# Kernel optimization log

Hardware: AMD Instinct MI355X
Metric: run time of the kernel (lower is better)

Reference implementation:

```python
import jax, jax.numpy as jnp
import numpy as np

INPUT_DIM = 1024; HIDDEN_DIM = 1024; OUTPUT_DIM = 1024
NUM_UNITS = 256; SPARSITY = 0.5
MOTOR = min(HIDDEN_DIM, NUM_UNITS - 4)      # 252 motor (output) neurons
REMAIN = NUM_UNITS - MOTOR                  # 4
COMMAND = max(int(0.4 * REMAIN), 1)         # 1 command neuron
INTER = REMAIN - COMMAND                    # 3 inter neurons
LAYERS = [(INPUT_DIM, INTER), (INTER, COMMAND), (COMMAND, MOTOR)]
B, T = 64, 1024
TS = 1.0  # timespans=None -> unit time step

# NCP-style fixed sparsity masks on ff1/ff2 weights (time_a/time_b unmasked, as in ncps CfCCell)
_rng = np.random.default_rng(0)
MASKS = [jnp.asarray((_rng.random((din + dh, dh)) < (1.0 - SPARSITY)).astype(np.float32)) for din, dh in LAYERS]

PARAM_NAMES = []
for _i in range(3):
    for _n in ('ff1', 'ff2', 'ta', 'tb'):
        PARAM_NAMES += [f'l{_i}_{_n}_w', f'l{_i}_{_n}_b']
PARAM_NAMES += ['hproj_w', 'hproj_b', 'oproj_w', 'oproj_b']


def setup_inputs() -> dict:
    key = jax.random.key(0)
    inp = {'x': jax.random.normal(jax.random.fold_in(key, 100), (B, T, INPUT_DIM), jnp.float32)}
    k = 0
    for i, (din, dh) in enumerate(LAYERS):
        cat = din + dh
        s = 1.0 / np.sqrt(cat)
        for name in ('ff1', 'ff2', 'ta', 'tb'):
            inp[f'l{i}_{name}_w'] = jax.random.uniform(jax.random.fold_in(key, k), (cat, dh), jnp.float32, -s, s); k += 1
            inp[f'l{i}_{name}_b'] = jnp.zeros((dh,), jnp.float32)
    sh = 1.0 / np.sqrt(MOTOR)
    inp['hproj_w'] = jax.random.uniform(jax.random.fold_in(key, 50), (MOTOR, HIDDEN_DIM), jnp.float32, -sh, sh)
    inp['hproj_b'] = jnp.zeros((HIDDEN_DIM,), jnp.float32)
    so = 1.0 / np.sqrt(HIDDEN_DIM)
    inp['oproj_w'] = jax.random.uniform(jax.random.fold_in(key, 51), (HIDDEN_DIM, OUTPUT_DIM), jnp.float32, -so, so)
    inp['oproj_b'] = jnp.zeros((OUTPUT_DIM,), jnp.float32)
    return inp


def _cfc_layer(xin, h, w1, b1, w2, b2, wa, ba, wb, bb, mask):
    # ncps CfCCell mode='default', no backbone: closed-form continuous-time update
    xh = jnp.concatenate([xin, h], axis=-1)
    ff1 = jnp.tanh(xh @ (w1 * mask) + b1)
    ff2 = jnp.tanh(xh @ (w2 * mask) + b2)
    t = jax.nn.sigmoid((xh @ wa + ba) * TS + (xh @ wb + bb))
    return ff1 * (1.0 - t) + t * ff2


def _forward(x, p):
    def step(carry, x_t):
        h0, h1, h2 = carry
        h0 = _cfc_layer(x_t, h0, p['l0_ff1_w'], p['l0_ff1_b'], p['l0_ff2_w'], p['l0_ff2_b'], p['l0_ta_w'], p['l0_ta_b'], p['l0_tb_w'], p['l0_tb_b'], MASKS[0])
        h1 = _cfc_layer(h0, h1, p['l1_ff1_w'], p['l1_ff1_b'], p['l1_ff2_w'], p['l1_ff2_b'], p['l1_ta_w'], p['l1_ta_b'], p['l1_tb_w'], p['l1_tb_b'], MASKS[1])
        h2 = _cfc_layer(h1, h2, p['l2_ff1_w'], p['l2_ff1_b'], p['l2_ff2_w'], p['l2_ff2_b'], p['l2_ta_w'], p['l2_ta_b'], p['l2_tb_w'], p['l2_tb_b'], MASKS[2])
        return (h0, h1, h2), None
    nb = x.shape[0]
    init = (jnp.zeros((nb, INTER), x.dtype), jnp.zeros((nb, COMMAND), x.dtype), jnp.zeros((nb, MOTOR), x.dtype))
    (h0, h1, h2), _ = jax.lax.scan(step, init, jnp.swapaxes(x, 0, 1))  # scan over time
    hx = jnp.concatenate([h0, h1, h2], axis=-1)  # (B, 256) full liquid state
    out = (h2 @ p['hproj_w'] + p['hproj_b']) @ p['oproj_w'] + p['oproj_b']  # motor -> hidden -> output
    return out, hx


def reference(x, l0_ff1_w, l0_ff1_b, l0_ff2_w, l0_ff2_b, l0_ta_w, l0_ta_b, l0_tb_w, l0_tb_b, l1_ff1_w, l1_ff1_b, l1_ff2_w, l1_ff2_b, l1_ta_w, l1_ta_b, l1_tb_w, l1_tb_b, l2_ff1_w, l2_ff1_b, l2_ff2_w, l2_ff2_b, l2_ta_w, l2_ta_b, l2_tb_w, l2_tb_b, hproj_w, hproj_b, oproj_w, oproj_b):
    p = dict(locals())
    x = p.pop('x')
    return _forward(x, p)
```

## Files before the change

kernel.cpp:

```cpp
#include <hip/hip_runtime.h>
#include <stdint.h>

static constexpr uint32_t OFF_MASK  = 0;
static constexpr uint32_t OFF_HID   = 0;
static constexpr uint32_t OFF_W0XT  = 66844;
static constexpr uint32_t OFF_W0H   = 76060;
static constexpr uint32_t OFF_B0    = 76088;
static constexpr uint32_t OFF_W1    = 76100;
static constexpr uint32_t OFF_B1    = 76112;
static constexpr uint32_t OFF_WH2   = 76116;
static constexpr uint32_t OFF_WH1   = 174420;
static constexpr uint32_t OFF_B2    = 175188;
static constexpr uint32_t OFF_XPART = 175948;
static constexpr uint32_t OFF_H2F   = 765772;

struct U128 { uint64_t lo, hi; };
__device__ inline U128 mul128(U128 a, U128 b) {
    U128 r; r.lo = a.lo * b.lo;
    r.hi = a.hi * b.lo + a.lo * b.hi + __umul64hi(a.lo, b.lo);
    return r;
}
__device__ inline U128 add128(U128 a, U128 b) {
    U128 r; r.lo = a.lo + b.lo; r.hi = a.hi + b.hi + (r.lo < b.lo); return r;
}
__device__ inline U128 pcg_mult() { U128 m; m.lo = 0x4385df649fccf645ull; m.hi = 0x2360ed051fc65da4ull; return m; }
__device__ inline void pcg_step(U128& st, U128 inc) { st = add128(mul128(st, pcg_mult()), inc); }

__device__ void pcg_init_np(U128& st, U128& inc) {
    const uint32_t IA = 0x43b0d7e5u, MA = 0x931e8875u, IB = 0x8b51f9ddu, MB = 0x58f38dedu;
    const uint32_t ML = 0xca01f9ddu, MR = 0x4973f715u;
    uint32_t hc = IA;
    auto hmix = [&](uint32_t val) -> uint32_t {
        val ^= hc; hc *= MA; val *= hc; val ^= val >> 16; return val;
    };
    auto mixf = [&](uint32_t x, uint32_t y) -> uint32_t {
        uint32_t r = (x * ML) - (y * MR); r ^= r >> 16; return r;
    };
    uint32_t pool[4];
    for (int i = 0; i < 4; i++) pool[i] = hmix(0u);
    for (int s = 0; s < 4; s++)
        for (int d = 0; d < 4; d++)
            if (s != d) pool[d] = mixf(pool[d], hmix(pool[s]));
    uint32_t hb = IB;
    uint32_t s32[8];
    for (int i = 0; i < 8; i++) {
        uint32_t dv = pool[i & 3];
        dv ^= hb; hb *= MB; dv *= hb; dv ^= dv >> 16;
        s32[i] = dv;
    }
    uint64_t w[4];
    for (int k = 0; k < 4; k++)
        w[k] = (uint64_t)s32[2 * k] | ((uint64_t)s32[2 * k + 1] << 32);
    U128 initstate; initstate.hi = w[0]; initstate.lo = w[1];
    inc.lo = (w[3] << 1) | 1ull;
    inc.hi = (w[2] << 1) | (w[3] >> 63);
    st.lo = 0; st.hi = 0;
    pcg_step(st, inc);
    st = add128(st, initstate);
    pcg_step(st, inc);
}
__device__ inline uint64_t pcg_draw(U128& st, U128 inc) {
    pcg_step(st, inc);
    uint64_t x = st.hi ^ st.lo;
    uint32_t rot = (uint32_t)(st.hi >> 58);
    return (x >> rot) | (x << ((64u - rot) & 63u));
}
__device__ void pcg_advance(U128& st, U128 inc, uint64_t delta) {
    U128 am; am.lo = 1; am.hi = 0;
    U128 ap; ap.lo = 0; ap.hi = 0;
    U128 cm = pcg_mult(), cp = inc;
    while (delta) {
        if (delta & 1) { am = mul128(am, cm); ap = add128(mul128(ap, cm), cp); }
        U128 cm1 = cm; cm1.lo += 1; cm1.hi += (cm1.lo == 0);
        cp = mul128(cm1, cp);
        cm = mul128(cm, cm);
        delta >>= 1;
    }
    st = add128(mul128(st, am), ap);
}

__global__ __launch_bounds__(256) void gen_masks(float* __restrict__ mask) {
    const int tid = threadIdx.x;
    U128 s, inc; pcg_init_np(s, inc);
    pcg_advance(s, inc, (uint64_t)tid * 262u);
    uint32_t base = (uint32_t)tid * 262u;
    for (uint32_t q = 0; q < 262u; q++) {
        uint64_t o = pcg_draw(s, inc);
        uint32_t idx = base + q;
        if (idx < 66841u) mask[idx] = (o >> 63) ? 0.0f : 1.0f;
    }
}

__global__ __launch_bounds__(256) void prep_weights(
    const float* f1w0, const float* f2w0, const float* taw0, const float* tbw0,
    const float* f1b0, const float* f2b0, const float* tab0, const float* tbb0,
    const float* f1w1, const float* f2w1, const float* taw1, const float* tbw1,
    const float* f1b1, const float* f2b1, const float* tab1, const float* tbb1,
    const float* f1w2, const float* f2w2, const float* taw2, const float* tbw2,
    const float* f1b2, const float* f2b2, const float* tab2, const float* tbb2,
    float* ws)
{
    const float* mask = ws + OFF_MASK;
    uint32_t id = blockIdx.x * 256u + threadIdx.x;
    if (id < 98304u) {
        uint32_t m = id / 32768u, r = id % 32768u;
        uint32_t q = r / 1024u, r2 = r % 1024u, jp = r2 >> 2, c = r2 & 3u;
        uint32_t p = q * 4u + c;
        auto wv = [&](uint32_t k) -> float {
            if (m == 0u) return f1w2[k * 252u + jp] * mask[3085u + k * 252u + jp];
            if (m == 1u) return f2w2[k * 252u + jp] * mask[3085u + k * 252u + jp];
            return taw2[k * 252u + jp] + tbw2[k * 252u + jp];
        };
        float a = 0.0f, bb = 0.0f;
        if (jp < 252u && p < 126u) { a = wv(1u + 2u * p); bb = wv(2u + 2u * p); }
        union { uint32_t u; _Float16 h[2]; } pk;
        pk.h[0] = (_Float16)a; pk.h[1] = (_Float16)bb;
        ((uint32_t*)ws)[OFF_WH2 + id] = pk.u;
        return;
    }
    uint32_t t = id - 98304u;
    if (t < 768u) {
        uint32_t mm = t / 256u, jp = t % 256u;
        float v = 0.0f;
        if (jp < 252u) {
            if (mm == 0u)      v = f1w2[jp] * mask[3085u + jp];
            else if (mm == 1u) v = f2w2[jp] * mask[3085u + jp];
            else               v = taw2[jp] + tbw2[jp];
        }
        ws[OFF_WH1 + t] = v;
        return;
    }
    t -= 768u;
    if (t < 9216u) {
        uint32_t c = t / 1024u, k = t % 1024u, m = c / 3u, cc = c % 3u;
        float v;
        if (m == 0u)      v = f1w0[k * 3u + cc] * mask[k * 3u + cc];
        else if (m == 1u) v = f2w0[k * 3u + cc] * mask[k * 3u + cc];
        else              v = taw0[k * 3u + cc] + tbw0[k * 3u + cc];
        ws[OFF_W0XT + c * 1024u + k] = v;
        return;
    }
    t -= 9216u;
    if (t < 27u) {
        uint32_t i = t / 9u, c = t % 9u, m = c / 3u, cc = c % 3u, k = 1024u + i;
        float v;
        if (m == 0u)      v = f1w0[k * 3u + cc] * mask[k * 3u + cc];
        else if (m == 1u) v = f2w0[k * 3u + cc] * mask[k * 3u + cc];
        else              v = taw0[k * 3u + cc] + tbw0[k * 3u + cc];
        ws[OFF_W0H + t] = v;
        return;
    }
    t -= 27u;
    if (t < 9u) {
        uint32_t m = t / 3u, cc = t % 3u;
        ws[OFF_B0 + t] = (m == 0u) ? f1b0[cc] : (m == 1u) ? f2b0[cc] : (tab0[cc] + tbb0[cc]);
        return;
    }
    t -= 9u;
    if (t < 12u) {
        uint32_t i = t / 3u, m = t % 3u;
        float v;
        if (m == 0u)      v = f1w1[i] * mask[3081u + i];
        else if (m == 1u) v = f2w1[i] * mask[3081u + i];
        else              v = taw1[i] + tbw1[i];
        ws[OFF_W1 + t] = v;
        return;
    }
    t -= 12u;
    if (t < 3u) {
        ws[OFF_B1 + t] = (t == 0u) ? f1b1[0] : (t == 1u) ? f2b1[0] : (tab1[0] + tbb1[0]);
        return;
    }
    t -= 3u;
    if (t < 756u) {
        uint32_t m = t / 252u, j = t % 252u;
        ws[OFF_B2 + t] = (m == 0u) ? f1b2[j] : (m == 1u) ? f2b2[j] : (tab2[j] + tbb2[j]);
        return;
    }
}

__global__ __launch_bounds__(256) void prepass(const float* __restrict__ x,
                                               const float* __restrict__ w0xt,
                                               float* __restrict__ xpart)
{
    size_t r = (size_t)blockIdx.x * 256u + threadIdx.x;
    const float4* xr = (const float4*)(x + r * 1024u);
    float acc[9] = {0, 0, 0, 0, 0, 0, 0, 0, 0};
    for (int q = 0; q < 256; q++) {
        float4 xv = xr[q];
        #pragma unroll
        for (int c = 0; c < 9; c++) {
            float4 wv = ((const float4*)(w0xt + c * 1024))[q];
            acc[c] += xv.x * wv.x + xv.y * wv.y + xv.z * wv.z + xv.w * wv.w;
        }
    }
    #pragma unroll
    for (int c = 0; c < 9; c++) xpart[r * 9u + c] = acc[c];
}

__device__ inline float dot2u(uint32_t w, uint32_t h, float acc) {
#if __has_builtin(__builtin_amdgcn_fdot2)
    typedef _Float16 h2v __attribute__((ext_vector_type(2)));
    union { uint32_t u; h2v v; } a, b;
    a.u = w; b.u = h;
    return __builtin_amdgcn_fdot2(a.v, b.v, acc, false);
#else
    union { uint32_t u; _Float16 s[2]; } a, b;
    a.u = w; b.u = h;
    return acc + (float)a.s[0] * (float)b.s[0] + (float)a.s[1] * (float)b.s[1];
#endif
}

__device__ inline float fsig(float x) { return 1.0f / (1.0f + __expf(-x)); }
__device__ inline float ftanh(float x) { float e = __expf(2.0f * x); return 1.0f - 2.0f / (e + 1.0f); }

__global__ __launch_bounds__(512, 1) void seq_kernel(
    const float* __restrict__ xpart, const uint32_t* __restrict__ wh2,
    const float* __restrict__ b2g, const float* __restrict__ wh1g,
    const float* __restrict__ w0h_g, const float* __restrict__ b0_g,
    const float* __restrict__ w1_g, const float* __restrict__ b1_g,
    float* __restrict__ hx, float* __restrict__ h2f)
{
    __shared__ alignas(16) _Float16 hbuf[2][256];
    __shared__ float part[3][256];
    const int tid = threadIdx.x;
    const int j = tid & 255;
    const int ks = tid >> 8;
    const int b = blockIdx.x;
    const bool owner = (ks == 0);
    const bool wr = owner && (j < 252);

    if (tid < 256) { hbuf[0][tid] = (_Float16)0.0f; hbuf[1][tid] = (_Float16)0.0f; }

    float w0h[27], b0[9], w1[12], b1[3];
    #pragma unroll
    for (int i = 0; i < 27; i++) w0h[i] = w0h_g[i];
    #pragma unroll
    for (int i = 0; i < 9; i++) b0[i] = b0_g[i];
    #pragma unroll
    for (int i = 0; i < 12; i++) w1[i] = w1_g[i];
    #pragma unroll
    for (int i = 0; i < 3; i++) b1[i] = b1_g[i];
    const int jc = (j < 252) ? j : 0;
    const float bj0 = b2g[jc], bj1 = b2g[252 + jc], bj2 = b2g[504 + jc];
    const float wh1a = wh1g[j], wh1b = wh1g[256 + j], wh1c = wh1g[512 + j];

    uint4 W0[16], W1[16], W2[16];
    const uint4* wq = (const uint4*)wh2;
    #pragma unroll
    for (int q = 0; q < 16; q++) W0[q] = wq[(0 * 32 + ks * 16 + q) * 256 + j];
    #pragma unroll
    for (int q = 0; q < 16; q++) W1[q] = wq[(1 * 32 + ks * 16 + q) * 256 + j];
    #pragma unroll
    for (int q = 0; q < 16; q++) W2[q] = wq[(2 * 32 + ks * 16 + q) * 256 + j];

    float h0a = 0, h0b = 0, h0c = 0, h1 = 0, h2r = 0;
    const float* xp = xpart + (size_t)b * 9216u;
    float xpc[9];
    #pragma unroll
    for (int c = 0; c < 9; c++) xpc[c] = xp[c];
    __syncthreads();

    for (int t = 0; t < 1024; t++) {
        float v[9];
        #pragma unroll
        for (int c = 0; c < 9; c++)
            v[c] = xpc[c] + b0[c] + h0a * w0h[c] + h0b * w0h[9 + c] + h0c * w0h[18 + c];
        if (t < 1023) {
            #pragma unroll
            for (int c = 0; c < 9; c++) xpc[c] = xp[(t + 1) * 9 + c];
        }
        float f10 = ftanh(v[0]), f11 = ftanh(v[1]), f12 = ftanh(v[2]);
        float f20 = ftanh(v[3]), f21 = ftanh(v[4]), f22 = ftanh(v[5]);
        float s0 = fsig(v[6]), s1 = fsig(v[7]), s2 = fsig(v[8]);
        float n0 = f10 * (1.0f - s0) + s0 * f20;
        float n1 = f11 * (1.0f - s1) + s1 * f21;
        float n2 = f12 * (1.0f - s2) + s2 * f22;
        float u0 = b1[0] + n0 * w1[0] + n1 * w1[3] + n2 * w1[6] + h1 * w1[9];
        float u1 = b1[1] + n0 * w1[1] + n1 * w1[4] + n2 * w1[7] + h1 * w1[10];
        float u2 = b1[2] + n0 * w1[2] + n1 * w1[5] + n2 * w1[8] + h1 * w1[11];
        float g1 = ftanh(u0), g2 = ftanh(u1), gs = fsig(u2);
        float h1n = g1 * (1.0f - gs) + gs * g2;
        h0a = n0; h0b = n1; h0c = n2; h1 = h1n;

        const uint4* xq = (const uint4*)hbuf[t & 1];
        float am0[2] = { 0, 0 }, am1[2] = { 0, 0 }, am2[2] = { 0, 0 };
        #pragma unroll
        for (int q = 0; q < 16; q++) {
            uint4 h4 = xq[ks * 16 + q];
            const int s = q & 1;
            am0[s] = dot2u(W0[q].x, h4.x, am0[s]);
            am0[s] = dot2u(W0[q].y, h4.y, am0[s]);
            am0[s] = dot2u(W0[q].z, h4.z, am0[s]);
            am0[s] = dot2u(W0[q].w, h4.w, am0[s]);
            am1[s] = dot2u(W1[q].x, h4.x, am1[s]);
            am1[s] = dot2u(W1[q].y, h4.y, am1[s]);
            am1[s] = dot2u(W1[q].z, h4.z, am1[s]);
            am1[s] = dot2u(W1[q].w, h4.w, am1[s]);
            am2[s] = dot2u(W2[q].x, h4.x, am2[s]);
            am2[s] = dot2u(W2[q].y, h4.y, am2[s]);
            am2[s] = dot2u(W2[q].z, h4.z, am2[s]);
            am2[s] = dot2u(W2[q].w, h4.w, am2[s]);
        }
        float a0 = am0[0] + am0[1];
        float a1 = am1[0] + am1[1];
        float a2 = am2[0] + am2[1];
        if (!owner) { part[0][j] = a0; part[1][j] = a1; part[2][j] = a2; }
        __syncthreads();
        if (owner) {
            a0 += part[0][j] + h1n * wh1a;
            a1 += part[1][j] + h1n * wh1b;
            a2 += part[2][j] + h1n * wh1c;
            float ff1 = ftanh(a0 + bj0), ff2 = ftanh(a1 + bj1), tg = fsig(a2 + bj2);
            float h2n = ff1 * (1.0f - tg) + tg * ff2;
            if (j < 252) { hbuf[(t & 1) ^ 1][j] = (_Float16)h2n; h2r = h2n; }
        }
        __syncthreads();
    }
    if (wr) { h2f[b * 252 + j] = h2r; hx[b * 256 + 4 + j] = h2r; }
    if (tid == 0) { hx[b * 256 + 0] = h0a; hx[b * 256 + 1] = h0b; hx[b * 256 + 2] = h0c; hx[b * 256 + 3] = h1; }
}

__global__ __launch_bounds__(256) void proj1(const float* __restrict__ h2f,
                                             const float* __restrict__ hw,
                                             const float* __restrict__ hb,
                                             float* __restrict__ hid)
{
    int c = blockIdx.x * 256 + threadIdx.x;
    int b = blockIdx.y;
    float acc = hb[c];
    const float* h2 = h2f + b * 252;
    #pragma unroll 4
    for (int k = 0; k < 252; k++) acc += h2[k] * hw[k * 1024 + c];
    hid[b * 1024 + c] = acc;
}

__global__ __launch_bounds__(256) void proj2(const float* __restrict__ hid,
                                             const float* __restrict__ ow,
                                             const float* __restrict__ ob,
                                             float* __restrict__ outp)
{
    int c = blockIdx.x * 256 + threadIdx.x;
    int b = blockIdx.y;
    float acc = ob[c];
    const float* hr = hid + b * 1024;
    #pragma unroll 4
    for (int k = 0; k < 1024; k++) acc += hr[k] * ow[k * 1024 + c];
    outp[b * 1024 + c] = acc;
}

extern "C" void kernel_launch(void* const* d_in, const int* in_sizes, int n_in,
                              void* d_out, int out_size, void* d_ws, size_t ws_size,
                              hipStream_t stream) {
    const float* x = (const float*)d_in[0];
    const float* l0_ff1_w = (const float*)d_in[1];
    const float* l0_ff1_b = (const float*)d_in[2];
    const float* l0_ff2_w = (const float*)d_in[3];
    const float* l0_ff2_b = (const float*)d_in[4];
    const float* l0_ta_w  = (const float*)d_in[5];
    const float* l0_ta_b  = (const float*)d_in[6];
    const float* l0_tb_w  = (const float*)d_in[7];
    const float* l0_tb_b  = (const float*)d_in[8];
    const float* l1_ff1_w = (const float*)d_in[9];
    const float* l1_ff1_b = (const float*)d_in[10];
    const float* l1_ff2_w = (const float*)d_in[11];
    const float* l1_ff2_b = (const float*)d_in[12];
    const float* l1_ta_w  = (const float*)d_in[13];
    const float* l1_ta_b  = (const float*)d_in[14];
    const float* l1_tb_w  = (const float*)d_in[15];
    const float* l1_tb_b  = (const float*)d_in[16];
    const float* l2_ff1_w = (const float*)d_in[17];
    const float* l2_ff1_b = (const float*)d_in[18];
    const float* l2_ff2_w = (const float*)d_in[19];
    const float* l2_ff2_b = (const float*)d_in[20];
    const float* l2_ta_w  = (const float*)d_in[21];
    const float* l2_ta_b  = (const float*)d_in[22];
    const float* l2_tb_w  = (const float*)d_in[23];
    const float* l2_tb_b  = (const float*)d_in[24];
    const float* hproj_w  = (const float*)d_in[25];
    const float* hproj_b  = (const float*)d_in[26];
    const float* oproj_w  = (const float*)d_in[27];
    const float* oproj_b  = (const float*)d_in[28];
    (void)in_sizes; (void)n_in; (void)out_size; (void)ws_size;

    float* ws = (float*)d_ws;
    uint32_t* wsu = (uint32_t*)d_ws;
    float* out = (float*)d_out;

    hipLaunchKernelGGL(gen_masks, dim3(1), dim3(256), 0, stream, ws + OFF_MASK);
    hipLaunchKernelGGL(prep_weights, dim3(427), dim3(256), 0, stream,
                       l0_ff1_w, l0_ff2_w, l0_ta_w, l0_tb_w,
                       l0_ff1_b, l0_ff2_b, l0_ta_b, l0_tb_b,
                       l1_ff1_w, l1_ff2_w, l1_ta_w, l1_tb_w,
                       l1_ff1_b, l1_ff2_b, l1_ta_b, l1_tb_b,
                       l2_ff1_w, l2_ff2_w, l2_ta_w, l2_tb_w,
                       l2_ff1_b, l2_ff2_b, l2_ta_b, l2_tb_b,
                       ws);
    hipLaunchKernelGGL(prepass, dim3(256), dim3(256), 0, stream,
                       x, ws + OFF_W0XT, ws + OFF_XPART);
    hipLaunchKernelGGL(seq_kernel, dim3(64), dim3(512), 0, stream,
                       ws + OFF_XPART, wsu + OFF_WH2, ws + OFF_B2, ws + OFF_WH1,
                       ws + OFF_W0H, ws + OFF_B0, ws + OFF_W1, ws + OFF_B1,
                       out + 65536, ws + OFF_H2F);
    hipLaunchKernelGGL(proj1, dim3(4, 64), dim3(256), 0, stream,
                       ws + OFF_H2F, hproj_w, hproj_b, ws + OFF_HID);
    hipLaunchKernelGGL(proj2, dim3(4, 64), dim3(256), 0, stream,
                       ws + OFF_HID, oproj_w, oproj_b, out);
}
```

Baseline: 2.327 ms.

## Split K within each wavefront and reduce via lane shuffle, dropping one barrier

The recurrent kernel now maps each wavefront to 32 output columns, with the two 32-lane halves each covering half of the 256-long hidden dimension. Partial sums are combined with a cross-lane xor shuffle instead of a shared-memory exchange. This removes one __syncthreads per time step and the LDS partial buffer, and the hidden vector is loaded into registers up front. The weight prep kernel is reordered to match the new per-lane layout, and empty asm statements pin the 48 weight vectors in VGPRs, which raises register pressure.

```diff
diff --git a/kernel.cpp b/kernel.cpp
--- a/kernel.cpp
+++ b/kernel.cpp
@@ -103,9 +103,13 @@
     const float* mask = ws + OFF_MASK;
     uint32_t id = blockIdx.x * 256u + threadIdx.x;
     if (id < 98304u) {
-        uint32_t m = id / 32768u, r = id % 32768u;
-        uint32_t q = r / 1024u, r2 = r % 1024u, jp = r2 >> 2, c = r2 & 3u;
-        uint32_t p = q * 4u + c;
+        uint32_t lin = id >> 2, cc = id & 3u;
+        uint32_t m = lin / 8192u, rem = lin % 8192u;
+        uint32_t q = rem / 512u, r2 = rem % 512u;
+        uint32_t w = r2 / 64u, l = r2 % 64u;
+        uint32_t kh = l >> 5, c = l & 31u;
+        uint32_t p = kh * 64u + q * 4u + cc;
+        uint32_t jp = w * 32u + c;
         auto wv = [&](uint32_t k) -> float {
             if (m == 0u) return f1w2[k * 252u + jp] * mask[3085u + k * 252u + jp];
             if (m == 1u) return f2w2[k * 252u + jp] * mask[3085u + k * 252u + jp];
@@ -115,7 +119,7 @@
         if (jp < 252u && p < 126u) { a = wv(1u + 2u * p); bb = wv(2u + 2u * p); }
         union { uint32_t u; _Float16 h[2]; } pk;
         pk.h[0] = (_Float16)a; pk.h[1] = (_Float16)bb;
-        ((uint32_t*)ws)[OFF_WH2 + id] = pk.u;
+        ((uint32_t*)ws)[OFF_WH2 + lin * 4u + cc] = pk.u;
         return;
     }
     uint32_t t = id - 98304u;
@@ -222,13 +226,13 @@
     float* __restrict__ hx, float* __restrict__ h2f)
 {
     __shared__ alignas(16) _Float16 hbuf[2][256];
-    __shared__ float part[3][256];
     const int tid = threadIdx.x;
-    const int j = tid & 255;
-    const int ks = tid >> 8;
+    const int w = tid >> 6;
+    const int l = tid & 63;
+    const int kh = l >> 5;
+    const int col = w * 32 + (l & 31);
     const int b = blockIdx.x;
-    const bool owner = (ks == 0);
-    const bool wr = owner && (j < 252);
+    const bool wrlane = (kh == 0) && (col < 252);
 
     if (tid < 256) { hbuf[0][tid] = (_Float16)0.0f; hbuf[1][tid] = (_Float16)0.0f; }
 
@@ -241,18 +245,20 @@
     for (int i = 0; i < 12; i++) w1[i] = w1_g[i];
     #pragma unroll
     for (int i = 0; i < 3; i++) b1[i] = b1_g[i];
-    const int jc = (j < 252) ? j : 0;
+    const int jc = (col < 252) ? col : 0;
     const float bj0 = b2g[jc], bj1 = b2g[252 + jc], bj2 = b2g[504 + jc];
-    const float wh1a = wh1g[j], wh1b = wh1g[256 + j], wh1c = wh1g[512 + j];
-
-    uint4 W0[16], W1[16], W2[16];
+    const float wh1a = wh1g[col], wh1b = wh1g[256 + col], wh1c = wh1g[512 + col];
+
+    uint4 W[48];
     const uint4* wq = (const uint4*)wh2;
     #pragma unroll
-    for (int q = 0; q < 16; q++) W0[q] = wq[(0 * 32 + ks * 16 + q) * 256 + j];
-    #pragma unroll
-    for (int q = 0; q < 16; q++) W1[q] = wq[(1 * 32 + ks * 16 + q) * 256 + j];
-    #pragma unroll
-    for (int q = 0; q < 16; q++) W2[q] = wq[(2 * 32 + ks * 16 + q) * 256 + j];
+    for (int m = 0; m < 3; m++)
+        #pragma unroll
+        for (int q = 0; q < 16; q++)
+            W[m * 16 + q] = wq[(((m * 16 + q) * 8 + w) << 6) + l];
+    #pragma unroll
+    for (int i = 0; i < 48; i++)
+        asm volatile("" : "+v"(W[i].x), "+v"(W[i].y), "+v"(W[i].z), "+v"(W[i].w));
 
     float h0a = 0, h0b = 0, h0c = 0, h1 = 0, h2r = 0;
     const float* xp = xpart + (size_t)b * 9216u;
@@ -284,40 +290,45 @@
         h0a = n0; h0b = n1; h0c = n2; h1 = h1n;
 
         const uint4* xq = (const uint4*)hbuf[t & 1];
+        uint4 hq[16];
+        #pragma unroll
+        for (int q = 0; q < 16; q++) hq[q] = xq[kh * 16 + q];
         float am0[2] = { 0, 0 }, am1[2] = { 0, 0 }, am2[2] = { 0, 0 };
         #pragma unroll
         for (int q = 0; q < 16; q++) {
-            uint4 h4 = xq[ks * 16 + q];
+            uint4 h4 = hq[q];
             const int s = q & 1;
-            am0[s] = dot2u(W0[q].x, h4.x, am0[s]);
-            am0[s] = dot2u(W0[q].y, h4.y, am0[s]);
-            am0[s] = dot2u(W0[q].z, h4.z, am0[s]);
-            am0[s] = dot2u(W0[q].w, h4.w, am0[s]);
-            am1[s] = dot2u(W1[q].x, h4.x, am1[s]);
-            am1[s] = dot2u(W1[q].y, h4.y, am1[s]);
-            am1[s] = dot2u(W1[q].z, h4.z, am1[s]);
-            am1[s] = dot2u(W1[q].w, h4.w, am1[s]);
-            am2[s] = dot2u(W2[q].x, h4.x, am2[s]);
-            am2[s] = dot2u(W2[q].y, h4.y, am2[s]);
-            am2[s] = dot2u(W2[q].z, h4.z, am2[s]);
-            am2[s] = dot2u(W2[q].w, h4.w, am2[s]);
+            uint4 w0v = W[q];
+            am0[s] = dot2u(w0v.x, h4.x, am0[s]);
+            am0[s] = dot2u(w0v.y, h4.y, am0[s]);
+            am0[s] = dot2u(w0v.z, h4.z, am0[s]);
+            am0[s] = dot2u(w0v.w, h4.w, am0[s]);
+            uint4 w1v = W[16 + q];
+            am1[s] = dot2u(w1v.x, h4.x, am1[s]);
+            am1[s] = dot2u(w1v.y, h4.y, am1[s]);
+            am1[s] = dot2u(w1v.z, h4.z, am1[s]);
+            am1[s] = dot2u(w1v.w, h4.w, am1[s]);
+            uint4 w2v = W[32 + q];
+            am2[s] = dot2u(w2v.x, h4.x, am2[s]);
+            am2[s] = dot2u(w2v.y, h4.y, am2[s]);
+            am2[s] = dot2u(w2v.z, h4.z, am2[s]);
+            am2[s] = dot2u(w2v.w, h4.w, am2[s]);
         }
         float a0 = am0[0] + am0[1];
         float a1 = am1[0] + am1[1];
         float a2 = am2[0] + am2[1];
-        if (!owner) { part[0][j] = a0; part[1][j] = a1; part[2][j] = a2; }
+        a0 += __shfl_xor(a0, 32);
+        a1 += __shfl_xor(a1, 32);
+        a2 += __shfl_xor(a2, 32);
+        a0 += h1n * wh1a;
+        a1 += h1n * wh1b;
+        a2 += h1n * wh1c;
+        float ff1 = ftanh(a0 + bj0), ff2 = ftanh(a1 + bj1), tg = fsig(a2 + bj2);
+        float h2n = ff1 * (1.0f - tg) + tg * ff2;
+        if (wrlane) { hbuf[(t & 1) ^ 1][col] = (_Float16)h2n; h2r = h2n; }
         __syncthreads();
-        if (owner) {
-            a0 += part[0][j] + h1n * wh1a;
-            a1 += part[1][j] + h1n * wh1b;
-            a2 += part[2][j] + h1n * wh1c;
-            float ff1 = ftanh(a0 + bj0), ff2 = ftanh(a1 + bj1), tg = fsig(a2 + bj2);
-            float h2n = ff1 * (1.0f - tg) + tg * ff2;
-            if (j < 252) { hbuf[(t & 1) ^ 1][j] = (_Float16)h2n; h2r = h2n; }
-        }
-        __syncthreads();
-    }
-    if (wr) { h2f[b * 252 + j] = h2r; hx[b * 256 + 4 + j] = h2r; }
+    }
+    if (wrlane) { h2f[b * 252 + col] = h2r; hx[b * 256 + 4 + col] = h2r; }
     if (tid == 0) { hx[b * 256 + 0] = h0a; hx[b * 256 + 1] = h0b; hx[b * 256 + 2] = h0c; hx[b * 256 + 3] = h1; }
 }
 
```

Result: slower. 2.623 ms (+12.7%).
